# Performance work log

Measured on AMD Instinct MI355X. Metric: run time of the kernel, lower is better.

## Reference

```python
import jax, jax.numpy as jnp
import numpy as np

N = 4096          # nodes
F_IN = 1386       # txt_feat_len
NHID = 1024       # per-head hidden
NHEADS = 8
CODE = 64         # code_len
LRELU_ALPHA = 0.2
NEG_INF = -9e15


def _build_adj(x):
    # F.normalize + cosine sim, threshold 0.8, sign -> {0,1}, then symmetric D^-1/2 A D^-1/2
    norm = jnp.maximum(jnp.linalg.norm(x, axis=1, keepdims=True), 1e-12)
    xn = x / norm
    sim = xn @ xn.T                                  # (N,N)
    A = (sim >= 0.8).astype(x.dtype)                 # sign after thresholding
    rowsum = A.sum(axis=1)
    r = jnp.where(rowsum > 0, rowsum ** -0.5, 0.0)
    adj = r[:, None] * A * r[None, :]                # symmetric normalized
    return jax.lax.stop_gradient(adj)                # torch code detaches x / adj is non-diff


def _gat_head(x, W, a, adj, concat):
    # x: (N,Fin), W: (Fin,H), a: (2H,1)
    H = W.shape[1]
    Wh = x @ W                                        # (N,H)
    f1 = Wh @ a[:H]                                   # (N,1)
    f2 = Wh @ a[H:]                                   # (N,1)
    e = jax.nn.leaky_relu(f1 + f2.T, LRELU_ALPHA)     # (N,N) pairwise scores
    e = jnp.where(adj > 0, e, NEG_INF)
    att = jax.nn.softmax(e, axis=1)                   # masked softmax (dropout off: eval)
    h = att @ Wh                                      # (N,H)
    return jax.nn.elu(h) if concat else h


def setup_inputs() -> dict:
    key = jax.random.key(0)
    k = jax.random.split(key, 5)
    x = jax.random.normal(k[0], (N, F_IN), dtype=jnp.float32)
    s_in = 1.0 / np.sqrt(F_IN)
    W_att = jax.random.uniform(k[1], (NHEADS, F_IN, NHID), jnp.float32, -s_in, s_in)
    a_att = jax.random.uniform(k[2], (NHEADS, 2 * NHID, 1), jnp.float32, -0.1, 0.1)
    s_h = 1.0 / np.sqrt(NHEADS * NHID)
    W_out = jax.random.uniform(k[3], (NHEADS * NHID, CODE), jnp.float32, -s_h, s_h)
    a_out = jax.random.uniform(k[4], (2 * CODE, 1), jnp.float32, -0.1, 0.1)
    return {"x": x, "W_att": W_att, "a_att": a_att, "W_out": W_out, "a_out": a_out}


def reference(x, W_att, a_att, W_out, a_out):
    adj = _build_adj(x)
    # 8 concat heads, vmapped over the head axis
    heads = jax.vmap(lambda W, a: _gat_head(x, W, a, adj, True))(W_att, a_att)  # (8,N,NHID)
    h = jnp.transpose(heads, (1, 0, 2)).reshape(N, NHEADS * NHID)               # cat dim=1
    out = _gat_head(h, W_out, a_out, adj, False)                                # (N,CODE)
    code = jnp.tanh(1.0 * out)                                                   # alpha=1.0
    return code
```

## Files before the change

kernel.cpp:

```cpp
#include <hip/hip_runtime.h>
#include <hip/hip_bf16.h>
#include <stdint.h>
#include <math.h>


typedef __bf16 bf16x8 __attribute__((ext_vector_type(8)));
typedef float  f32x4  __attribute__((ext_vector_type(4)));
typedef unsigned short ushort8 __attribute__((ext_vector_type(8)));

#define AS1C(p) ((const __attribute__((address_space(1))) void*)(p))
#define AS3(p)  ((__attribute__((address_space(3))) void*)(p))

#define MODE_WH  0
#define MODE_SIM 1
#define MODE_F32 2

__device__ __forceinline__ float bfbits2f(unsigned short u) {
    return __uint_as_float(((unsigned)u) << 16);
}
__device__ __forceinline__ unsigned short f2bfbits(float v) {
    __hip_bfloat16 b = __float2bfloat16(v);
    return *(unsigned short*)&b;
}

__device__ __forceinline__ bool row_fast(const unsigned* __restrict__ mask,
                                         const unsigned* __restrict__ summ,
                                         int row)
{
    const uint4 s = *(const uint4*)(summ + row * 4);
    unsigned sw[4] = { s.x, s.y, s.z, s.w };
    const int wi = row >> 5;
    bool fast = (sw[wi >> 5] == (1u << (wi & 31)));
    sw[wi >> 5] = 0;
    fast = fast && !(sw[0] | sw[1] | sw[2] | sw[3]);
    return fast && (mask[row * 128 + wi] == (1u << (row & 31)));
}

template<int MODE>
__device__ __forceinline__ void gemm_body(
    __hip_bfloat16* __restrict__ As, __hip_bfloat16* __restrict__ Bs,
    int bx, int by,
    const __hip_bfloat16* __restrict__ A,
    const __hip_bfloat16* __restrict__ B,
    int lda, int ldb, int K,
    void* __restrict__ Cv, int ldc, int Nreal,
    const float* __restrict__ norms,
    unsigned* __restrict__ mask,
    unsigned* __restrict__ summary,
    __hip_bfloat16* __restrict__ hout)
{
    const int tid  = threadIdx.x;
    const int lane = tid & 63;
    const int wave = tid >> 6;
    const int m0   = bx * 128;
    const int n0   = by * 128;

    f32x4 acc[4][4];
#pragma unroll
    for (int i = 0; i < 4; ++i)
#pragma unroll
        for (int j = 0; j < 4; ++j)
#pragma unroll
            for (int k = 0; k < 4; ++k) acc[i][j][k] = 0.f;

    const int wm = wave >> 1, wn = wave & 1;
    const int q  = lane >> 4, ln = lane & 15;

    const int kIters = K >> 5;
    for (int kt = 0; kt < kIters; ++kt) {
        __syncthreads();
#pragma unroll
        for (int p = 0; p < 2; ++p) {
            const int t   = p * 256 + tid;
            const int row = t >> 2;
            const int kb  = (t & 3) ^ ((t >> 3) & 3);
            const __hip_bfloat16* ga = A + (long long)(m0 + row) * lda + kt * 32 + kb * 8;
            const __hip_bfloat16* gb = B + (long long)(n0 + row) * ldb + kt * 32 + kb * 8;
            __hip_bfloat16* sa = As + (p * 256 + wave * 64) * 8;
            __hip_bfloat16* sb = Bs + (p * 256 + wave * 64) * 8;
            __builtin_amdgcn_global_load_lds(AS1C(ga), AS3(sa), 16, 0, 0);
            __builtin_amdgcn_global_load_lds(AS1C(gb), AS3(sb), 16, 0, 0);
        }
        __syncthreads();

        bf16x8 afr[4], bfr[4];
#pragma unroll
        for (int rg = 0; rg < 4; ++rg) {
            const int r = wm * 64 + rg * 16 + ln;
            const int s = q ^ ((r >> 1) & 3);
            afr[rg] = *(const bf16x8*)(As + r * 32 + s * 8);
        }
#pragma unroll
        for (int cg = 0; cg < 4; ++cg) {
            const int r = wn * 64 + cg * 16 + ln;
            const int s = q ^ ((r >> 1) & 3);
            bfr[cg] = *(const bf16x8*)(Bs + r * 32 + s * 8);
        }
#pragma unroll
        for (int rg = 0; rg < 4; ++rg)
#pragma unroll
            for (int cg = 0; cg < 4; ++cg)
                acc[rg][cg] = __builtin_amdgcn_mfma_f32_16x16x32_bf16(
                    afr[rg], bfr[cg], acc[rg][cg], 0, 0, 0);
    }

#pragma unroll
    for (int rg = 0; rg < 4; ++rg) {
#pragma unroll
        for (int i = 0; i < 4; ++i) {
            const int row = m0 + wm * 64 + rg * 16 + q * 4 + i;
            bool fast = false;
            if (MODE == MODE_WH) fast = row_fast(mask, summary, row);
#pragma unroll
            for (int cg = 0; cg < 4; ++cg) {
                const int col = n0 + wn * 64 + cg * 16 + ln;
                const float v = acc[rg][cg][i];
                if (MODE == MODE_WH) {
                    if (fast) {
                        const float u = v > 0.f ? v : (__expf(v) - 1.f);
                        hout[(long long)row * 8192 + col] = __float2bfloat16(u);
                    } else {
                        __hip_bfloat16* C = (__hip_bfloat16*)Cv;
                        C[(long long)row * ldc + col] = __float2bfloat16(v);
                    }
                } else if (MODE == MODE_SIM) {
                    if (v >= 0.8f * norms[row] * norms[col]) {
                        atomicOr(&mask[row * 128 + (col >> 5)], 1u << (col & 31));
                        atomicOr(&summary[row * 4 + (col >> 10)], 1u << ((col >> 5) & 31));
                        atomicOr(&mask[col * 128 + (row >> 5)], 1u << (row & 31));
                        atomicOr(&summary[col * 4 + (row >> 10)], 1u << ((row >> 5) & 31));
                    }
                } else {
                    if (col < Nreal) {
                        float* C = (float*)Cv;
                        C[(long long)row * ldc + col] = v;
                    }
                }
            }
        }
    }
}

__global__ __launch_bounds__(256)
void prestage(const float* __restrict__ x,
              const float* __restrict__ W_att,
              const float* __restrict__ W_out,
              const float* __restrict__ a_att,
              __hip_bfloat16* __restrict__ x_bf,
              float* __restrict__ norms,
              __hip_bfloat16* __restrict__ Wt_bf,
              __hip_bfloat16* __restrict__ WoutT,
              float* __restrict__ wa)
{
    __shared__ float ts[32][33];
    __shared__ float red[4];
    const int id  = blockIdx.x;
    const int tid = threadIdx.x;

    if (id < 4096) {
        const int i = id;
        float ss = 0.f;
        for (int c = tid; c < 1408; c += 256) {
            float v = (c < 1386) ? x[(long long)i * 1386 + c] : 0.f;
            x_bf[(long long)i * 1408 + c] = __float2bfloat16(v);
            ss += v * v;
        }
        for (int off = 32; off; off >>= 1) ss += __shfl_down(ss, off);
        if ((tid & 63) == 0) red[tid >> 6] = ss;
        __syncthreads();
        if (tid == 0) norms[i] = fmaxf(sqrtf(red[0] + red[1] + red[2] + red[3]), 1e-12f);
        return;
    }
    if (id < 16384) {
        const float* s; __hip_bfloat16* d;
        int K, N, Kpad, Npad, k0, n0;
        if (id < 15360) {
            const int b = id - 4096;
            const int h = b / 1408, r = b % 1408;
            const int kx = r % 44, ny = r / 44;
            s = W_att + (long long)h * 1386 * 1024;
            d = Wt_bf + (long long)h * 1024 * 1408;
            K = 1386; N = 1024; Kpad = 1408; Npad = 1024;
            k0 = kx * 32; n0 = ny * 32;
        } else {
            const int r = id - 15360;
            s = W_out; d = WoutT;
            K = 8192; N = 64; Kpad = 8192; Npad = 128;
            k0 = (r & 255) * 32; n0 = (r >> 8) * 32;
        }
        const int tx = tid & 31, ty = tid >> 5;
#pragma unroll
        for (int i = 0; i < 4; ++i) {
            const int k = k0 + ty + i * 8;
            const int n = n0 + tx;
            ts[ty + i * 8][tx] = (k < K && n < N) ? s[(long long)k * N + n] : 0.f;
        }
        __syncthreads();
#pragma unroll
        for (int i = 0; i < 4; ++i) {
            const int n  = n0 + ty + i * 8;
            const int kk = k0 + tx;
            if (n < Npad && kk < Kpad)
                d[(long long)n * Kpad + kk] = __float2bfloat16(ts[tx][ty + i * 8]);
        }
        return;
    }
    {
        const int b = id - 16384;
        const int h = b / 352, r = b % 352;
        const int wave = tid >> 6, lane = tid & 63;
        const int c = r * 4 + wave;
        float s1 = 0.f, s2 = 0.f;
        if (c < 1386) {
            const float* wr = W_att + ((long long)h * 1386 + c) * 1024;
            const float* a1 = a_att + (long long)h * 2048;
            const float* a2 = a1 + 1024;
#pragma unroll
            for (int t = 0; t < 16; ++t) {
                const int j = lane + t * 64;
                const float w = wr[j];
                s1 += w * a1[j];
                s2 += w * a2[j];
            }
        }
        for (int off = 32; off; off >>= 1) { s1 += __shfl_down(s1, off); s2 += __shfl_down(s2, off); }
        if (lane == 0) {
            wa[(h * 2 + 0) * 1408 + c] = s1;
            wa[(h * 2 + 1) * 1408 + c] = s2;
        }
    }
}

__global__ __launch_bounds__(256, 2)
void simf12(const __hip_bfloat16* __restrict__ x_bf,
            const float* __restrict__ norms,
            unsigned* __restrict__ mask,
            unsigned* __restrict__ summ,
            const float* __restrict__ x,
            const float* __restrict__ wa,
            float2* __restrict__ f12)
{
    __shared__ __align__(16) __hip_bfloat16 As[128 * 32];
    __shared__ __align__(16) __hip_bfloat16 Bs[128 * 32];
    const int id = blockIdx.x;

    if (id < 528) {
        int t = (int)((sqrtf(8.f * id + 1.f) - 1.f) * 0.5f);
        while (t * (t + 1) / 2 > id) --t;
        while ((t + 1) * (t + 2) / 2 <= id) ++t;
        const int by = t, bx = id - t * (t + 1) / 2;
        gemm_body<MODE_SIM>(As, Bs, bx, by, x_bf, x_bf, 1408, 1408, 1408,
                            nullptr, 0, 0, norms, mask, summ, nullptr);
        return;
    }
    {
        const int b    = id - 528;
        const int wave = threadIdx.x >> 6, lane = threadIdx.x & 63;
        const int i    = b * 4 + wave;
        float s[16];
#pragma unroll
        for (int j = 0; j < 16; ++j) s[j] = 0.f;
        const float* xr = x + (long long)i * 1386;
        for (int c = lane; c < 1386; c += 64) {
            const float v = xr[c];
#pragma unroll
            for (int j = 0; j < 16; ++j) s[j] += v * wa[j * 1408 + c];
        }
#pragma unroll
        for (int j = 0; j < 16; ++j)
            for (int off = 32; off; off >>= 1) s[j] += __shfl_down(s[j], off);
        if (lane == 0) {
#pragma unroll
            for (int h = 0; h < 8; ++h)
                f12[(long long)h * 4096 + i] = make_float2(s[h * 2], s[h * 2 + 1]);
        }
    }
}

__global__ __launch_bounds__(256, 2)
void whh(const __hip_bfloat16* __restrict__ x_bf,
         const __hip_bfloat16* __restrict__ Wt_bf,
         __hip_bfloat16* __restrict__ Wh,
         __hip_bfloat16* __restrict__ hout,
         unsigned* __restrict__ mask,
         unsigned* __restrict__ summ)
{
    __shared__ __align__(16) __hip_bfloat16 As[128 * 32];
    __shared__ __align__(16) __hip_bfloat16 Bs[128 * 32];
    const int id = blockIdx.x;
    const int z  = id >> 8;
    const int r  = id & 255;
    const int bx = r & 31, by = r >> 5;
    gemm_body<MODE_WH>(As, Bs, bx, by,
                       x_bf, Wt_bf + (long long)z * 1024 * 1408,
                       1408, 1408, 1408,
                       Wh + (long long)z * 4096 * 1024, 1024, 1024,
                       nullptr, mask, summ, hout + (long long)z * 1024);
}

__global__ __launch_bounds__(256, 2)
void out_gemm(const __hip_bfloat16* __restrict__ hout,
              const __hip_bfloat16* __restrict__ WoutT,
              float* __restrict__ parts)
{
    __shared__ __align__(16) __hip_bfloat16 As[128 * 32];
    __shared__ __align__(16) __hip_bfloat16 Bs[128 * 32];
    const int z = blockIdx.z;
    gemm_body<MODE_F32>(As, Bs, blockIdx.x, 0,
                        hout + z * 512, WoutT + z * 512, 8192, 8192, 512,
                        parts + (long long)z * 4096 * 64, 64, 64,
                        nullptr, nullptr, nullptr, nullptr);
}

__global__ __launch_bounds__(256)
void attn_fix(const __hip_bfloat16* __restrict__ Wh,
              const float2* __restrict__ f12,
              const unsigned* __restrict__ mask,
              const unsigned* __restrict__ summary,
              __hip_bfloat16* __restrict__ hout)
{
    const int wv   = threadIdx.x >> 6;
    const int lane = threadIdx.x & 63;
    const int i    = blockIdx.x * 4 + wv;
    const int h    = blockIdx.y;
    if (row_fast(mask, summary, i)) return;

    const float2* f = f12 + (long long)h * 4096;
    const float f1 = f[i].x;
    const unsigned* mrow = mask + (long long)i * 128;
    const __hip_bfloat16* WhH = Wh + (long long)h * 4096 * 1024;
    const uint4 sm = *(const uint4*)(summary + (long long)i * 4);
    unsigned sw[4] = { sm.x, sm.y, sm.z, sm.w };
    const int cbase = lane * 16;

    float m = -INFINITY, l = 0.f;
    float acc[16];
#pragma unroll
    for (int k = 0; k < 16; ++k) acc[k] = 0.f;

#pragma unroll
    for (int s = 0; s < 4; ++s) {
        unsigned sb = sw[s];
        while (sb) {
            const int w = s * 32 + __builtin_ctz(sb);
            sb &= sb - 1;
            unsigned bits = mrow[w];
            while (bits) {
                const int j = w * 32 + __builtin_ctz(bits);
                bits &= bits - 1;
                float e = f1 + f[j].y;
                e = e > 0.f ? e : 0.2f * e;
                float wgt;
                if (e > m) {
                    const float sc = __expf(m - e);
                    l *= sc;
#pragma unroll
                    for (int k = 0; k < 16; ++k) acc[k] *= sc;
                    m = e; wgt = 1.f;
                } else {
                    wgt = __expf(e - m);
                }
                l += wgt;
                const ushort8* p = (const ushort8*)(WhH + (long long)j * 1024 + cbase);
                const ushort8 w0 = p[0], w1 = p[1];
#pragma unroll
                for (int k = 0; k < 8; ++k) acc[k]     += wgt * bfbits2f(w0[k]);
#pragma unroll
                for (int k = 0; k < 8; ++k) acc[k + 8] += wgt * bfbits2f(w1[k]);
            }
        }
    }
    const float inv = 1.f / l;
    ushort8 o0, o1;
#pragma unroll
    for (int k = 0; k < 8; ++k) {
        float v = acc[k] * inv;     v = v > 0.f ? v : (__expf(v) - 1.f); o0[k] = f2bfbits(v);
        float u = acc[k + 8] * inv; u = u > 0.f ? u : (__expf(u) - 1.f); o1[k] = f2bfbits(u);
    }
    ushort8* op = (ushort8*)(hout + (long long)i * 8192 + (long long)h * 1024 + cbase);
    op[0] = o0; op[1] = o1;
}

__global__ void out_reduce_f(const float* __restrict__ parts,
                             const float* __restrict__ a_out,
                             float* __restrict__ Cout,
                             float* __restrict__ f1o,
                             float* __restrict__ f2o)
{
    const int i = blockIdx.x, c = threadIdx.x;
    float v = 0.f;
#pragma unroll
    for (int z = 0; z < 16; ++z) v += parts[(long long)z * 4096 * 64 + (long long)i * 64 + c];
    Cout[(long long)i * 64 + c] = v;
    float s1 = v * a_out[c];
    float s2 = v * a_out[64 + c];
    for (int off = 32; off; off >>= 1) { s1 += __shfl_down(s1, off); s2 += __shfl_down(s2, off); }
    if (c == 0) { f1o[i] = s1; f2o[i] = s2; }
}

__global__ __launch_bounds__(256)
void attn_out(const float* __restrict__ Cout,
              const float* __restrict__ f1o,
              const float* __restrict__ f2o,
              const unsigned* __restrict__ mask,
              const unsigned* __restrict__ summary,
              float* __restrict__ out)
{
    const int wv = threadIdx.x >> 6;
    const int c  = threadIdx.x & 63;
    const int i  = blockIdx.x * 4 + wv;
    const float f1 = f1o[i];
    const unsigned* mrow = mask + (long long)i * 128;
    const uint4 sm = *(const uint4*)(summary + (long long)i * 4);
    unsigned sw[4] = { sm.x, sm.y, sm.z, sm.w };
    float m = -INFINITY, l = 0.f, acc = 0.f;
#pragma unroll
    for (int s = 0; s < 4; ++s) {
        unsigned sb = sw[s];
        while (sb) {
            const int w = s * 32 + __builtin_ctz(sb);
            sb &= sb - 1;
            unsigned bits = mrow[w];
            while (bits) {
                const int j = w * 32 + __builtin_ctz(bits);
                bits &= bits - 1;
                float e = f1 + f2o[j];
                e = e > 0.f ? e : 0.2f * e;
                float wgt;
                if (e > m) { const float sc = __expf(m - e); l *= sc; acc *= sc; m = e; wgt = 1.f; }
                else       { wgt = __expf(e - m); }
                l += wgt;
                acc += wgt * Cout[(long long)j * 64 + c];
            }
        }
    }
    out[(long long)i * 64 + c] = tanhf(acc / l);
}

extern "C" void kernel_launch(void* const* d_in, const int* in_sizes, int n_in,
                              void* d_out, int out_size, void* d_ws, size_t ws_size,
                              hipStream_t stream)
{
    (void)in_sizes; (void)n_in; (void)out_size;
    const float* x     = (const float*)d_in[0];
    const float* W_att = (const float*)d_in[1];
    const float* a_att = (const float*)d_in[2];
    const float* W_out = (const float*)d_in[3];
    const float* a_out = (const float*)d_in[4];
    float* out = (float*)d_out;

    char* ws = (char*)d_ws;
    size_t off = 0;
    auto alloc = [&](size_t bytes) -> void* {
        void* p = ws + off;
        off += (bytes + 255) & ~(size_t)255;
        return p;
    };

    __hip_bfloat16* x_bf  = (__hip_bfloat16*)alloc(4096LL * 1408 * 2);
    __hip_bfloat16* Wt_bf = (__hip_bfloat16*)alloc(8LL * 1024 * 1408 * 2);
    __hip_bfloat16* WoutT = (__hip_bfloat16*)alloc(128LL * 8192 * 2);
    float*          norms = (float*)alloc(4096 * 4);
    unsigned*       mask  = (unsigned*)alloc(4096LL * 128 * 4);
    unsigned*       summ  = (unsigned*)alloc(4096LL * 4 * 4);
    float*          wa    = (float*)alloc(16LL * 1408 * 4);
    float2*         f12   = (float2*)alloc(8LL * 4096 * 8);
    float*          parts = (float*)alloc(16LL * 4096 * 64 * 4);
    float*          Cout  = (float*)alloc(4096LL * 64 * 4);
    float*          f1o   = (float*)alloc(4096 * 4);
    float*          f2o   = (float*)alloc(4096 * 4);
    __hip_bfloat16* Wh    = (__hip_bfloat16*)alloc(8LL * 4096 * 1024 * 2);
    __hip_bfloat16* hout  = (__hip_bfloat16*)alloc(8LL * 4096 * 1024 * 2);
    if (off > ws_size) return;

    hipMemsetAsync(mask, 0, 4096LL * 128 * 4 + 4096LL * 4 * 4, stream);

    prestage<<<19200, 256, 0, stream>>>(x, W_att, W_out, a_att,
                                        x_bf, norms, Wt_bf, WoutT, wa);

    simf12<<<1552, 256, 0, stream>>>(x_bf, norms, mask, summ, x, wa, f12);

    whh<<<2048, 256, 0, stream>>>(x_bf, Wt_bf, Wh, hout, mask, summ);

    attn_fix<<<dim3(1024, 8), 256, 0, stream>>>(Wh, f12, mask, summ, hout);

    out_gemm<<<dim3(32, 1, 16), 256, 0, stream>>>(hout, WoutT, parts);

    out_reduce_f<<<4096, 64, 0, stream>>>(parts, a_out, Cout, f1o, f2o);
    attn_out<<<1024, 256, 0, stream>>>(Cout, f1o, f2o, mask, summ, out);
}
```

Measured before the change: 332.5 us.

## Rebalance prestage work across kernels and fast-path trivial output rows

Removes the memset by having the per-row norm blocks clear mask and summary rows themselves. Moves the large W_att transpose-to-bf16 work out of the first kernel and into the similarity kernel, so it runs alongside the sim GEMM tiles. Merges out_reduce into a 4-wave-per-block finisher that writes tanh directly for rows flagged by row_fast, and the attention output kernel skips those rows. This cuts launch and serialization overhead at the cost of heavier mixed-role kernels, and it relies on row_fast (not shown) being correct.

```diff
diff --git a/kernel.cpp b/kernel.cpp
--- a/kernel.cpp
+++ b/kernel.cpp
@@ -142,15 +142,16 @@
 }
 
 __global__ __launch_bounds__(256)
-void prestage(const float* __restrict__ x,
-              const float* __restrict__ W_att,
-              const float* __restrict__ W_out,
-              const float* __restrict__ a_att,
-              __hip_bfloat16* __restrict__ x_bf,
-              float* __restrict__ norms,
-              __hip_bfloat16* __restrict__ Wt_bf,
-              __hip_bfloat16* __restrict__ WoutT,
-              float* __restrict__ wa)
+void stage1(const float* __restrict__ x,
+            const float* __restrict__ W_att,
+            const float* __restrict__ W_out,
+            const float* __restrict__ a_att,
+            __hip_bfloat16* __restrict__ x_bf,
+            float* __restrict__ norms,
+            __hip_bfloat16* __restrict__ WoutT,
+            float* __restrict__ wa,
+            unsigned* __restrict__ mask,
+            unsigned* __restrict__ summ)
 {
     __shared__ float ts[32][33];
     __shared__ float red[4];
@@ -159,6 +160,8 @@
 
     if (id < 4096) {
         const int i = id;
+        if (tid < 128) mask[i * 128 + tid] = 0;
+        else if (tid < 132) summ[i * 4 + (tid - 128)] = 0;
         float ss = 0.f;
         for (int c = tid; c < 1408; c += 256) {
             float v = (c < 1386) ? x[(long long)i * 1386 + c] : 0.f;
@@ -171,42 +174,27 @@
         if (tid == 0) norms[i] = fmaxf(sqrtf(red[0] + red[1] + red[2] + red[3]), 1e-12f);
         return;
     }
-    if (id < 16384) {
-        const float* s; __hip_bfloat16* d;
-        int K, N, Kpad, Npad, k0, n0;
-        if (id < 15360) {
-            const int b = id - 4096;
-            const int h = b / 1408, r = b % 1408;
-            const int kx = r % 44, ny = r / 44;
-            s = W_att + (long long)h * 1386 * 1024;
-            d = Wt_bf + (long long)h * 1024 * 1408;
-            K = 1386; N = 1024; Kpad = 1408; Npad = 1024;
-            k0 = kx * 32; n0 = ny * 32;
-        } else {
-            const int r = id - 15360;
-            s = W_out; d = WoutT;
-            K = 8192; N = 64; Kpad = 8192; Npad = 128;
-            k0 = (r & 255) * 32; n0 = (r >> 8) * 32;
-        }
+    if (id < 5120) {
+        const int r  = id - 4096;
+        const int k0 = (r & 255) * 32, n0 = (r >> 8) * 32;
         const int tx = tid & 31, ty = tid >> 5;
 #pragma unroll
         for (int i = 0; i < 4; ++i) {
             const int k = k0 + ty + i * 8;
             const int n = n0 + tx;
-            ts[ty + i * 8][tx] = (k < K && n < N) ? s[(long long)k * N + n] : 0.f;
+            ts[ty + i * 8][tx] = (n < 64) ? W_out[(long long)k * 64 + n] : 0.f;
         }
         __syncthreads();
 #pragma unroll
         for (int i = 0; i < 4; ++i) {
             const int n  = n0 + ty + i * 8;
             const int kk = k0 + tx;
-            if (n < Npad && kk < Kpad)
-                d[(long long)n * Kpad + kk] = __float2bfloat16(ts[tx][ty + i * 8]);
+            WoutT[(long long)n * 8192 + kk] = __float2bfloat16(ts[tx][ty + i * 8]);
         }
         return;
     }
     {
-        const int b = id - 16384;
+        const int b = id - 5120;
         const int h = b / 352, r = b % 352;
         const int wave = tid >> 6, lane = tid & 63;
         const int c = r * 4 + wave;
@@ -224,7 +212,7 @@
             }
         }
         for (int off = 32; off; off >>= 1) { s1 += __shfl_down(s1, off); s2 += __shfl_down(s2, off); }
-        if (lane == 0) {
+        if (lane == 0 && c < 1386) {
             wa[(h * 2 + 0) * 1408 + c] = s1;
             wa[(h * 2 + 1) * 1408 + c] = s2;
         }
@@ -232,10 +220,12 @@
 }
 
 __global__ __launch_bounds__(256, 2)
-void simf12(const __hip_bfloat16* __restrict__ x_bf,
+void stage2(const __hip_bfloat16* __restrict__ x_bf,
             const float* __restrict__ norms,
             unsigned* __restrict__ mask,
             unsigned* __restrict__ summ,
+            const float* __restrict__ W_att,
+            __hip_bfloat16* __restrict__ Wt_bf,
             const float* __restrict__ x,
             const float* __restrict__ wa,
             float2* __restrict__ f12)
@@ -253,8 +243,34 @@
                             nullptr, 0, 0, norms, mask, summ, nullptr);
         return;
     }
+    if (id < 11792) {
+        float (*ts)[33] = (float(*)[33])As;
+        const int tid = threadIdx.x;
+        const int b = id - 528;
+        const int h = b / 1408, r = b % 1408;
+        const int kx = r % 44, ny = r / 44;
+        const float* s = W_att + (long long)h * 1386 * 1024;
+        __hip_bfloat16* d = Wt_bf + (long long)h * 1024 * 1408;
+        const int k0 = kx * 32, n0 = ny * 32;
+        const int tx = tid & 31, ty = tid >> 5;
+#pragma unroll
+        for (int i = 0; i < 4; ++i) {
+            const int k = k0 + ty + i * 8;
+            const int n = n0 + tx;
+            ts[ty + i * 8][tx] = (k < 1386) ? s[(long long)k * 1024 + n] : 0.f;
+        }
+        __syncthreads();
+#pragma unroll
+        for (int i = 0; i < 4; ++i) {
+            const int n  = n0 + ty + i * 8;
+            const int kk = k0 + tx;
+            if (kk < 1408)
+                d[(long long)n * 1408 + kk] = __float2bfloat16(ts[tx][ty + i * 8]);
+        }
+        return;
+    }
     {
-        const int b    = id - 528;
+        const int b    = id - 11792;
         const int wave = threadIdx.x >> 6, lane = threadIdx.x & 63;
         const int i    = b * 4 + wave;
         float s[16];
@@ -381,13 +397,19 @@
     op[0] = o0; op[1] = o1;
 }
 
-__global__ void out_reduce_f(const float* __restrict__ parts,
-                             const float* __restrict__ a_out,
-                             float* __restrict__ Cout,
-                             float* __restrict__ f1o,
-                             float* __restrict__ f2o)
-{
-    const int i = blockIdx.x, c = threadIdx.x;
+__global__ __launch_bounds__(256)
+void out_finish(const float* __restrict__ parts,
+                const float* __restrict__ a_out,
+                float* __restrict__ Cout,
+                float* __restrict__ f1o,
+                float* __restrict__ f2o,
+                const unsigned* __restrict__ mask,
+                const unsigned* __restrict__ summ,
+                float* __restrict__ out)
+{
+    const int wv = threadIdx.x >> 6;
+    const int c  = threadIdx.x & 63;
+    const int i  = blockIdx.x * 4 + wv;
     float v = 0.f;
 #pragma unroll
     for (int z = 0; z < 16; ++z) v += parts[(long long)z * 4096 * 64 + (long long)i * 64 + c];
@@ -396,19 +418,22 @@
     float s2 = v * a_out[64 + c];
     for (int off = 32; off; off >>= 1) { s1 += __shfl_down(s1, off); s2 += __shfl_down(s2, off); }
     if (c == 0) { f1o[i] = s1; f2o[i] = s2; }
+    if (row_fast(mask, summ, i))
+        out[(long long)i * 64 + c] = tanhf(v);
 }
 
 __global__ __launch_bounds__(256)
-void attn_out(const float* __restrict__ Cout,
-              const float* __restrict__ f1o,
-              const float* __restrict__ f2o,
-              const unsigned* __restrict__ mask,
-              const unsigned* __restrict__ summary,
-              float* __restrict__ out)
+void attn_out_fix(const float* __restrict__ Cout,
+                  const float* __restrict__ f1o,
+                  const float* __restrict__ f2o,
+                  const unsigned* __restrict__ mask,
+                  const unsigned* __restrict__ summary,
+                  float* __restrict__ out)
 {
     const int wv = threadIdx.x >> 6;
     const int c  = threadIdx.x & 63;
     const int i  = blockIdx.x * 4 + wv;
+    if (row_fast(mask, summary, i)) return;
     const float f1 = f1o[i];
     const unsigned* mrow = mask + (long long)i * 128;
     const uint4 sm = *(const uint4*)(summary + (long long)i * 4);
@@ -473,12 +498,11 @@
     __hip_bfloat16* hout  = (__hip_bfloat16*)alloc(8LL * 4096 * 1024 * 2);
     if (off > ws_size) return;
 
-    hipMemsetAsync(mask, 0, 4096LL * 128 * 4 + 4096LL * 4 * 4, stream);
-
-    prestage<<<19200, 256, 0, stream>>>(x, W_att, W_out, a_att,
-                                        x_bf, norms, Wt_bf, WoutT, wa);
-
-    simf12<<<1552, 256, 0, stream>>>(x_bf, norms, mask, summ, x, wa, f12);
+    stage1<<<7936, 256, 0, stream>>>(x, W_att, W_out, a_att,
+                                     x_bf, norms, WoutT, wa, mask, summ);
+
+    stage2<<<12816, 256, 0, stream>>>(x_bf, norms, mask, summ,
+                                      W_att, Wt_bf, x, wa, f12);
 
     whh<<<2048, 256, 0, stream>>>(x_bf, Wt_bf, Wh, hout, mask, summ);
 
@@ -486,6 +510,7 @@
 
     out_gemm<<<dim3(32, 1, 16), 256, 0, stream>>>(hout, WoutT, parts);
 
-    out_reduce_f<<<4096, 64, 0, stream>>>(parts, a_out, Cout, f1o, f2o);
-    attn_out<<<1024, 256, 0, stream>>>(Cout, f1o, f2o, mask, summ, out);
-}
+    out_finish<<<1024, 256, 0, stream>>>(parts, a_out, Cout, f1o, f2o,
+                                         mask, summ, out);
+    attn_out_fix<<<1024, 256, 0, stream>>>(Cout, f1o, f2o, mask, summ, out);
+}
```

Measured after the change: 309.5 us. 1.07x faster.
